# Kernel tuning notes

Hardware: AMD Instinct MI355X
Metric: run time of the kernel (lower is better)

The kernel has to match this reference:

```python
import jax, jax.numpy as jnp
import numpy as np

N_NODES = 20000
N_EDGES = 160000
N_GRAPHS = 64
EMB_DIM = 16
N_BASIS = 16
MAX_RADIUS = 5.0
MUL_IN = 8   # output_size: multiplicity of scalar atom features
MUL_OUT = 4  # multiplicity per output irrep (4x0e + 4x1o + 4x2e -> dim 36)
W_NUMEL = 3 * MUL_IN * MUL_IN * MUL_OUT  # 768 per-edge tensor-product weights


def setup_inputs() -> dict:
    key = jax.random.key(0)
    ks = jax.random.split(key, 16)
    pos = jax.random.normal(ks[0], (N_NODES, 3), jnp.float32) * 3.0
    A = jax.random.randint(ks[1], (N_NODES,), 0, 10)
    batch = jnp.sort(jax.random.randint(ks[2], (N_NODES,), 0, N_GRAPHS))
    edge_src = jax.random.randint(ks[3], (N_EDGES,), 0, N_NODES)
    edge_dst = jax.random.randint(ks[4], (N_EDGES,), 0, N_NODES)
    edge_shifts = jnp.zeros((N_EDGES, 3), jnp.float32)
    cell = jnp.broadcast_to(jnp.eye(3, dtype=jnp.float32) * 10.0, (N_GRAPHS, 3, 3))
    emb_table = jax.random.normal(ks[5], (10, EMB_DIM), jnp.float32)
    fit_w1 = jax.random.normal(ks[6], (EMB_DIM, 64), jnp.float32) * (2.0 / EMB_DIM) ** 0.5
    fit_b1 = jnp.zeros((64,), jnp.float32)
    fit_w2 = jax.random.normal(ks[7], (64, 32), jnp.float32) * (2.0 / 64.0) ** 0.5
    fit_b2 = jnp.zeros((32,), jnp.float32)
    fit_w3 = jax.random.normal(ks[8], (32, MUL_IN), jnp.float32) * (2.0 / 32.0) ** 0.5
    fit_b3 = jnp.zeros((MUL_IN,), jnp.float32)
    fc_w1 = jax.random.normal(ks[9], (N_BASIS, 64), jnp.float32)
    fc_w2 = jax.random.normal(ks[10], (64, 64), jnp.float32)
    fc_w3 = jax.random.normal(ks[11], (64, 64), jnp.float32)
    fc_w4 = jax.random.normal(ks[12], (64, W_NUMEL), jnp.float32)
    return dict(pos=pos, A=A, batch=batch, edge_src=edge_src, edge_dst=edge_dst,
                edge_shifts=edge_shifts, cell=cell, emb_table=emb_table,
                fit_w1=fit_w1, fit_b1=fit_b1, fit_w2=fit_w2, fit_b2=fit_b2,
                fit_w3=fit_w3, fit_b3=fit_b3,
                fc_w1=fc_w1, fc_w2=fc_w2, fc_w3=fc_w3, fc_w4=fc_w4)


def _forward(pos, edge_shifts, cell, emb_table, fit_w1, fit_b1, fit_w2, fit_b2,
             fit_w3, fit_b3, fc_w1, fc_w2, fc_w3, fc_w4, A, batch, edge_src, edge_dst):
    E = edge_src.shape[0]
    # edge vectors with periodic shifts
    shift = jnp.einsum('ni,nij->nj', edge_shifts, cell[batch[edge_src]])
    ev = pos[edge_dst] - pos[edge_src] + shift                     # [E,3]
    r = jnp.sqrt(jnp.sum(ev * ev, axis=1))                         # [E]
    v = ev / jnp.maximum(r, 1e-9)[:, None]
    x, y, z = v[:, 0], v[:, 1], v[:, 2]
    # spherical harmonics lmax=2, normalize=True, 'component' normalization (e3nn order)
    sh0 = jnp.ones_like(x)                                         # [E]
    sh1 = jnp.sqrt(3.0) * jnp.stack([y, z, x], axis=-1)            # [E,3]
    s15 = jnp.sqrt(15.0); s5 = jnp.sqrt(5.0)
    sh2 = jnp.stack([s15 * x * y, s15 * y * z, (s5 / 2.0) * (3.0 * z * z - 1.0),
                     s15 * x * z, (s15 / 2.0) * (x * x - y * y)], axis=-1)  # [E,5]
    # node scalar features: embedding + fitnet MLP (SiLU)
    h = jax.nn.silu(emb_table[A] @ fit_w1 + fit_b1)
    h = jax.nn.silu(h @ fit_w2 + fit_b2)
    Ai = h @ fit_w3 + fit_b3                                       # [N, MUL_IN]
    # soft_one_hot_linspace(gaussian, cutoff=True) * sqrt(n_basis)
    centers = jnp.linspace(0.0, MAX_RADIUS, N_BASIS + 2)[1:-1]
    step = centers[1] - centers[0]
    rb = jnp.exp(-(((r[:, None] - centers) / step) ** 2)) / 1.12 * jnp.sqrt(jnp.float32(N_BASIS))
    # radial net -> per-edge tensor-product weights (e3nn FullyConnectedNet style, no bias)
    g = jax.nn.silu(rb @ fc_w1 / jnp.sqrt(jnp.float32(N_BASIS)))
    g = jax.nn.silu(g @ fc_w2 / 8.0)
    g = jax.nn.silu(g @ fc_w3 / 8.0)
    w = (g @ fc_w4 / 8.0).reshape(E, 3, MUL_IN, MUL_IN, MUL_OUT)   # [E,3 paths,u,v,w]
    # FullTensorProduct(Ai_src, sh) then FullyConnectedTensorProduct(., Ai_dst) with
    # per-edge weights; scalar x irrep paths factorize: out_l[e,w,m] = S_l[e,w]*sh_l[e,m]
    P = Ai[edge_src][:, :, None] * Ai[edge_dst][:, None, :]        # [E,u,v]
    S = jnp.einsum('euv,eluvw->elw', P, w) / jnp.float32(MUL_IN)   # path norm 1/sqrt(u*v)
    out0 = S[:, 0, :] * sh0[:, None]                               # [E,4]
    out1 = (S[:, 1, :, None] * sh1[:, None, :]).reshape(E, MUL_OUT * 3)
    out2 = (S[:, 2, :, None] * sh2[:, None, :]).reshape(E, MUL_OUT * 5)
    ef = jnp.concatenate([out0, out1, out2], axis=-1)              # [E,36]
    # scatter-mean to destination nodes
    cnt = jnp.clip(jax.ops.segment_sum(jnp.ones((E,), ef.dtype), edge_dst,
                                       num_segments=N_NODES), 1.0)
    return jax.ops.segment_sum(ef, edge_dst, num_segments=N_NODES) / cnt[:, None]


def reference(pos, A, batch, edge_src, edge_dst, edge_shifts, cell, emb_table,
              fit_w1, fit_b1, fit_w2, fit_b2, fit_w3, fit_b3,
              fc_w1, fc_w2, fc_w3, fc_w4):
    return _forward(pos, edge_shifts, cell, emb_table, fit_w1, fit_b1, fit_w2,
                    fit_b2, fit_w3, fit_b3, fc_w1, fc_w2, fc_w3, fc_w4,
                    A, batch, edge_src, edge_dst)
```

## Files before the change

kernel.cpp:

```cpp
#include <hip/hip_runtime.h>
#include <math.h>

#define N_NODES 20000
#define N_EDGES 160000

#define NBINS   512
#define BINS1   513
#define RMAX    7.5f

static const size_t OFF_T   = 0;
static const size_t OFF_G   = OFF_T   + (size_t)100 * 64 * 12 * 4;
static const size_t OFF_SV  = OFF_G   + (size_t)64 * BINS1 * 4;
static const size_t OFF_NOFF= OFF_SV  + (size_t)100 * BINS1 * 12 * 4;
static const size_t OFF_NCNT= OFF_NOFF+ (size_t)(N_NODES + 1) * 4;
static const size_t OFF_RANK= OFF_NCNT+ (size_t)N_NODES * 4;
static const size_t OFF_CSR = OFF_RANK+ (size_t)N_EDGES * 4;

#define P1_T_BLOCKS  25
#define P1_G_BLOCKS  9
#define P1_H_BLOCKS  625
#define P1_GRID (P1_T_BLOCKS + P1_G_BLOCKS + P1_H_BLOCKS)
#define P2_SCAN_BLOCKS 79
#define P2_CHUNKS 9
#define P2_GRID (P2_SCAN_BLOCKS + 100 * P2_CHUNKS)

__device__ __forceinline__ float silu_f(float x) {
    return x / (1.0f + __expf(-x));
}

__global__ __launch_bounds__(256) void prep1_kernel(
        const float* __restrict__ emb,
        const float* __restrict__ fw1, const float* __restrict__ fb1,
        const float* __restrict__ fw2, const float* __restrict__ fb2,
        const float* __restrict__ fw3, const float* __restrict__ fb3,
        const float* __restrict__ fc_w1, const float* __restrict__ fc_w2,
        const float* __restrict__ fc_w3, const float* __restrict__ fc_w4,
        const int* __restrict__ edst,
        float* __restrict__ T, float* __restrict__ g_tT,
        int* __restrict__ cnt_i, int* __restrict__ rank_e) {
    __shared__ float smem[4096];
    int b = blockIdx.x;
    int tid = threadIdx.x;

    if (b < P1_T_BLOCKS) {
        float* h1s = smem;
        float* h2s = smem + 640;
        float* ai  = smem + 960;
        for (int idx = tid; idx < 640; idx += 256) {
            int t = idx >> 6, j = idx & 63;
            float acc = fb1[j];
            #pragma unroll
            for (int i = 0; i < 16; i++) acc += emb[t * 16 + i] * fw1[i * 64 + j];
            h1s[idx] = silu_f(acc);
        }
        __syncthreads();
        for (int idx = tid; idx < 320; idx += 256) {
            int t = idx >> 5, j = idx & 31;
            float acc = fb2[j];
            #pragma unroll
            for (int i = 0; i < 64; i++) acc += h1s[t * 64 + i] * fw2[i * 32 + j];
            h2s[idx] = silu_f(acc);
        }
        __syncthreads();
        if (tid < 80) {
            int t = tid >> 3, j = tid & 7;
            float acc = fb3[j];
            #pragma unroll
            for (int i = 0; i < 32; i++) acc += h2s[t * 32 + i] * fw3[i * 8 + j];
            ai[tid] = acc;
        }
        __syncthreads();

        int idx = b * 256 + tid;
        int pair = idx >> 6;
        int k = idx & 63;
        int ts = pair / 10, td = pair - ts * 10;
        float a[8], bb[8];
        #pragma unroll
        for (int i = 0; i < 8; i++) a[i] = ai[ts * 8 + i];
        #pragma unroll
        for (int i = 0; i < 8; i++) bb[i] = ai[td * 8 + i];
        float sv[12];
        #pragma unroll
        for (int i = 0; i < 12; i++) sv[i] = 0.0f;
        const float* wk = fc_w4 + k * 768;
        #pragma unroll 2
        for (int u = 0; u < 8; u++) {
            #pragma unroll
            for (int v = 0; v < 8; v++) {
                float ab = a[u] * bb[v];
                const float* wp = wk + u * 32 + v * 4;
                float4 w0 = *(const float4*)(wp);
                float4 w1 = *(const float4*)(wp + 256);
                float4 w2 = *(const float4*)(wp + 512);
                sv[0] += ab * w0.x; sv[1] += ab * w0.y; sv[2]  += ab * w0.z; sv[3]  += ab * w0.w;
                sv[4] += ab * w1.x; sv[5] += ab * w1.y; sv[6]  += ab * w1.z; sv[7]  += ab * w1.w;
                sv[8] += ab * w2.x; sv[9] += ab * w2.y; sv[10] += ab * w2.z; sv[11] += ab * w2.w;
            }
        }
        float* tp = T + pair * 768 + k * 12;
        #pragma unroll
        for (int j = 0; j < 12; j++) tp[j] = sv[j];
    } else if (b < P1_T_BLOCKS + P1_G_BLOCKS) {
        int lane = tid & 63;
        int wq = __builtin_amdgcn_readfirstlane(tid >> 6);
        int bin = (b - P1_T_BLOCKS) * 64 + lane;
        bool valid = (bin <= NBINS);
        float r = (float)bin * (RMAX / (float)NBINS);

        float rb[16];
        const float step = 5.0f / 17.0f;
        const float istep = 17.0f / 5.0f;
        const float rsc = 4.0f / 1.12f;
        #pragma unroll
        for (int i = 0; i < 16; i++) {
            float dd = (r - (float)(i + 1) * step) * istep;
            rb[i] = __expf(-dd * dd) * rsc;
        }

        #pragma unroll
        for (int jj = 0; jj < 16; jj++) {
            int j = wq * 16 + jj;
            float a0 = 0, a1 = 0, a2 = 0, a3 = 0;
            #pragma unroll
            for (int i = 0; i < 16; i += 4) {
                a0 += rb[i]     * fc_w1[(i)     * 64 + j];
                a1 += rb[i + 1] * fc_w1[(i + 1) * 64 + j];
                a2 += rb[i + 2] * fc_w1[(i + 2) * 64 + j];
                a3 += rb[i + 3] * fc_w1[(i + 3) * 64 + j];
            }
            smem[j * 64 + lane] = silu_f(((a0 + a1) + (a2 + a3)) * 0.25f);
        }
        __syncthreads();

        float acc[16];
        #pragma unroll
        for (int jj = 0; jj < 16; jj++) acc[jj] = 0.0f;
        #pragma unroll
        for (int c = 0; c < 4; c++) {
            float hc[16];
            #pragma unroll
            for (int i = 0; i < 16; i++) hc[i] = smem[(c * 16 + i) * 64 + lane];
            #pragma unroll
            for (int jj = 0; jj < 16; jj++) {
                int j = wq * 16 + jj;
                #pragma unroll
                for (int i = 0; i < 16; i++) acc[jj] += hc[i] * fc_w2[(c * 16 + i) * 64 + j];
            }
        }
        __syncthreads();
        #pragma unroll
        for (int jj = 0; jj < 16; jj++) smem[(wq * 16 + jj) * 64 + lane] = silu_f(acc[jj] * 0.125f);
        __syncthreads();

        #pragma unroll
        for (int jj = 0; jj < 16; jj++) acc[jj] = 0.0f;
        #pragma unroll
        for (int c = 0; c < 4; c++) {
            float hc[16];
            #pragma unroll
            for (int i = 0; i < 16; i++) hc[i] = smem[(c * 16 + i) * 64 + lane];
            #pragma unroll
            for (int jj = 0; jj < 16; jj++) {
                int j = wq * 16 + jj;
                #pragma unroll
                for (int i = 0; i < 16; i++) acc[jj] += hc[i] * fc_w3[(c * 16 + i) * 64 + j];
            }
        }
        if (valid) {
            #pragma unroll
            for (int jj = 0; jj < 16; jj++)
                g_tT[(size_t)(wq * 16 + jj) * BINS1 + bin] = silu_f(acc[jj] * 0.125f);
        }
    } else {
        int e = (b - P1_T_BLOCKS - P1_G_BLOCKS) * 256 + tid;
        if (e < N_EDGES) rank_e[e] = atomicAdd(&cnt_i[edst[e]], 1);
    }
}

__global__ __launch_bounds__(256) void prep2_kernel(
        const int* __restrict__ cnt_i, int* __restrict__ node_off,
        const float* __restrict__ T, const float* __restrict__ g_tT,
        float* __restrict__ sv_table) {
    __shared__ float smem[4096];
    int b = blockIdx.x;
    int tid = threadIdx.x;

    if (b < P2_SCAN_BLOCKS) {
        int* wred = (int*)smem;
        int* wsum = (int*)smem + 4;
        int lane = tid & 63, w = tid >> 6;
        int nbase = b * 256;
        int n = nbase + tid;
        int c = (n < N_NODES) ? cnt_i[n] : 0;

        int part = 0;
        for (int i = tid; i < nbase; i += 256) part += cnt_i[i];
        #pragma unroll
        for (int off = 1; off < 64; off <<= 1) part += __shfl_xor(part, off);
        if (lane == 0) wred[w] = part;

        int sc = c;
        #pragma unroll
        for (int off = 1; off < 64; off <<= 1) {
            int v2 = __shfl_up(sc, off);
            if (lane >= off) sc += v2;
        }
        if (lane == 63) wsum[w] = sc;
        __syncthreads();

        int base = wred[0] + wred[1] + wred[2] + wred[3];
        int wb = 0;
        #pragma unroll
        for (int i = 0; i < 4; i++) wb += (i < w) ? wsum[i] : 0;
        if (n < N_NODES) node_off[n] = base + wb + (sc - c);
        if (b == 0 && tid == 0) node_off[N_NODES] = N_EDGES;
        return;
    }

    int idx = b - P2_SCAN_BLOCKS;
    int pair = idx / P2_CHUNKS;
    int chunk = idx - pair * P2_CHUNKS;

    float* part = smem;
    float* Tlds = smem + 3328;

    const float* Tp = T + pair * 768;
    #pragma unroll
    for (int i = tid; i < 768; i += 256) Tlds[i] = Tp[i];
    __syncthreads();

    int lane = tid & 63;
    int wq = tid >> 6;
    int bin = chunk * 64 + lane;
    bool valid = (bin <= NBINS);
    int rb = valid ? bin : NBINS;

    float acc[12];
    #pragma unroll
    for (int j = 0; j < 12; j++) acc[j] = 0.0f;
    #pragma unroll
    for (int kk = 0; kk < 16; kk++) {
        int k = wq * 16 + kk;
        float g = g_tT[(size_t)k * BINS1 + rb];
        const float* Tl = Tlds + k * 12;
        #pragma unroll
        for (int j = 0; j < 12; j++) acc[j] += g * Tl[j];
    }

    float* pp = part + (size_t)wq * 64 * 13 + (size_t)lane * 13;
    #pragma unroll
    for (int j = 0; j < 12; j++) pp[j] = acc[j];
    __syncthreads();

    const float isc = 1.0f / 64.0f;
    float* svp = sv_table + (size_t)pair * BINS1 * 12 + (size_t)chunk * 64 * 12;
    #pragma unroll
    for (int i = 0; i < 3; i++) {
        int o = tid + 256 * i;
        int bl = o / 12;
        int j = o - bl * 12;
        if (chunk * 64 + bl <= NBINS) {
            float s = part[(size_t)0 * 832 + bl * 13 + j]
                    + part[(size_t)1 * 832 + bl * 13 + j]
                    + part[(size_t)2 * 832 + bl * 13 + j]
                    + part[(size_t)3 * 832 + bl * 13 + j];
            svp[o] = s * isc;
        }
    }
}

__global__ __launch_bounds__(256) void csr_kernel(
        const int* __restrict__ edst, const int* __restrict__ rank_e,
        const int* __restrict__ node_off, int* __restrict__ csr_eid) {
    int e = blockIdx.x * 256 + threadIdx.x;
    if (e >= N_EDGES) return;
    csr_eid[node_off[edst[e]] + rank_e[e]] = e;
}

__global__ __launch_bounds__(256) void gather_kernel(
        const float* __restrict__ pos, const int* __restrict__ batch,
        const int* __restrict__ esrc, const float* __restrict__ shifts,
        const float* __restrict__ cell, const int* __restrict__ A,
        const int* __restrict__ node_off, const int* __restrict__ csr_eid,
        const float* __restrict__ sv_table, float* __restrict__ out) {
    int t = blockIdx.x * 256 + threadIdx.x;
    if (t >= N_NODES * 8) return;
    int n = t >> 3;
    int q = t & 7;
    int beg = node_off[n], end = node_off[n + 1];

    float pdx = pos[n * 3 + 0], pdy = pos[n * 3 + 1], pdz = pos[n * 3 + 2];
    int Ad = A[n];

    const float S3  = 1.7320508075688772f;
    const float S15 = 3.8729833462074170f;
    const float S5  = 2.2360679774997896f;

    float acc[36];
    #pragma unroll
    for (int j = 0; j < 36; j++) acc[j] = 0.0f;

    for (int p = beg + q; p < end; p += 8) {
        int e = csr_eid[p];
        int s = esrc[e];
        int gb = batch[s];
        float t0 = shifts[e * 3 + 0], t1 = shifts[e * 3 + 1], t2 = shifts[e * 3 + 2];
        const float* C = cell + gb * 9;
        float shx = t0 * C[0] + t1 * C[3] + t2 * C[6];
        float shy = t0 * C[1] + t1 * C[4] + t2 * C[7];
        float shz = t0 * C[2] + t1 * C[5] + t2 * C[8];
        float ex = pdx - pos[s * 3 + 0] + shx;
        float ey = pdy - pos[s * 3 + 1] + shy;
        float ez = pdz - pos[s * 3 + 2] + shz;
        float r = sqrtf(ex * ex + ey * ey + ez * ez);
        float inv = 1.0f / fmaxf(r, 1e-9f);
        float x = ex * inv, y = ey * inv, z = ez * inv;

        float sv[12];
        if (r >= RMAX) {
            #pragma unroll
            for (int j = 0; j < 12; j++) sv[j] = 0.0f;
        } else {
            int pair = A[s] * 10 + Ad;
            float tt = r * ((float)NBINS / RMAX);
            int i = (int)tt;
            i = (i > NBINS - 1) ? (NBINS - 1) : i;
            float f = tt - (float)i;
            const float* r0 = sv_table + ((size_t)pair * BINS1 + i) * 12;
            #pragma unroll
            for (int j = 0; j < 12; j++) {
                float lo = r0[j], hi = r0[12 + j];
                sv[j] = lo + f * (hi - lo);
            }
        }

        float sh1v[3] = { S3 * y, S3 * z, S3 * x };
        float sh2v[5] = { S15 * x * y, S15 * y * z, 0.5f * S5 * (3.0f * z * z - 1.0f),
                          S15 * x * z, 0.5f * S15 * (x * x - y * y) };

        acc[0] += sv[0]; acc[1] += sv[1]; acc[2] += sv[2]; acc[3] += sv[3];
        #pragma unroll
        for (int w = 0; w < 4; w++) {
            float sw = sv[4 + w];
            #pragma unroll
            for (int j = 0; j < 3; j++) acc[4 + w * 3 + j] += sw * sh1v[j];
        }
        #pragma unroll
        for (int w = 0; w < 4; w++) {
            float sw = sv[8 + w];
            #pragma unroll
            for (int j = 0; j < 5; j++) acc[16 + w * 5 + j] += sw * sh2v[j];
        }
    }

    #pragma unroll
    for (int j = 0; j < 36; j++) {
        acc[j] += __shfl_xor(acc[j], 1);
        acc[j] += __shfl_xor(acc[j], 2);
        acc[j] += __shfl_xor(acc[j], 4);
    }

    if (q == 0) {
        float c = 1.0f / fmaxf((float)(end - beg), 1.0f);
        float4* o4 = (float4*)out + (size_t)n * 9;
        #pragma unroll
        for (int k = 0; k < 9; k++)
            o4[k] = make_float4(acc[k * 4 + 0] * c, acc[k * 4 + 1] * c,
                                acc[k * 4 + 2] * c, acc[k * 4 + 3] * c);
    }
}

extern "C" void kernel_launch(void* const* d_in, const int* in_sizes, int n_in,
                              void* d_out, int out_size, void* d_ws, size_t ws_size,
                              hipStream_t stream) {
    const float* pos    = (const float*)d_in[0];
    const int*   A      = (const int*)d_in[1];
    const int*   batch  = (const int*)d_in[2];
    const int*   esrc   = (const int*)d_in[3];
    const int*   edst   = (const int*)d_in[4];
    const float* shifts = (const float*)d_in[5];
    const float* cell   = (const float*)d_in[6];
    const float* emb    = (const float*)d_in[7];
    const float* fw1    = (const float*)d_in[8];
    const float* fb1    = (const float*)d_in[9];
    const float* fw2    = (const float*)d_in[10];
    const float* fb2    = (const float*)d_in[11];
    const float* fw3    = (const float*)d_in[12];
    const float* fb3    = (const float*)d_in[13];
    const float* fcw1   = (const float*)d_in[14];
    const float* fcw2   = (const float*)d_in[15];
    const float* fcw3   = (const float*)d_in[16];
    const float* fcw4   = (const float*)d_in[17];
    float* out = (float*)d_out;

    char* ws = (char*)d_ws;
    float* T       = (float*)(ws + OFF_T);
    float* g_tT    = (float*)(ws + OFF_G);
    float* sv_table= (float*)(ws + OFF_SV);
    int*   node_off= (int*)(ws + OFF_NOFF);
    int*   cnt_i   = (int*)(ws + OFF_NCNT);
    int*   rank_e  = (int*)(ws + OFF_RANK);
    int*   csr_eid = (int*)(ws + OFF_CSR);

    hipMemsetAsync(cnt_i, 0, (size_t)N_NODES * 4, stream);

    prep1_kernel<<<P1_GRID, 256, 0, stream>>>(emb, fw1, fb1, fw2, fb2, fw3, fb3,
                                              fcw1, fcw2, fcw3, fcw4, edst,
                                              T, g_tT, cnt_i, rank_e);
    prep2_kernel<<<P2_GRID, 256, 0, stream>>>(cnt_i, node_off, T, g_tT, sv_table);
    csr_kernel<<<(N_EDGES + 255) / 256, 256, 0, stream>>>(edst, rank_e, node_off, csr_eid);
    gather_kernel<<<(N_NODES * 8 + 255) / 256, 256, 0, stream>>>(
        pos, batch, esrc, shifts, cell, A, node_off, csr_eid, sv_table, out);
}
```

Measured before the change: 157.3 us.

## Stage per-edge source position and species into CSR order before gather

Replaces the CSR edge-id scatter with a staging kernel. Each edge's shifted source position and source species are written as a float4 at its sorted slot. The gather kernel then reads one contiguous float4 per edge instead of chasing edge id, source index, batch, cell, pos and A through indirect loads. Lanes per node also rise from 8 to 16, with one extra shuffle stage. In exchange the workspace write per edge grows to 16 bytes, and most lanes sit idle for nodes with few edges.

```diff
diff --git a/kernel.cpp b/kernel.cpp
--- a/kernel.cpp
+++ b/kernel.cpp
@@ -14,7 +14,7 @@
 static const size_t OFF_NOFF= OFF_SV  + (size_t)100 * BINS1 * 12 * 4;
 static const size_t OFF_NCNT= OFF_NOFF+ (size_t)(N_NODES + 1) * 4;
 static const size_t OFF_RANK= OFF_NCNT+ (size_t)N_NODES * 4;
-static const size_t OFF_CSR = OFF_RANK+ (size_t)N_EDGES * 4;
+static const size_t OFF_STG = OFF_RANK+ (size_t)N_EDGES * 4;
 
 #define P1_T_BLOCKS  25
 #define P1_G_BLOCKS  9
@@ -270,24 +270,38 @@
     }
 }
 
-__global__ __launch_bounds__(256) void csr_kernel(
-        const int* __restrict__ edst, const int* __restrict__ rank_e,
-        const int* __restrict__ node_off, int* __restrict__ csr_eid) {
+__global__ __launch_bounds__(256) void stage_kernel(
+        const float* __restrict__ pos, const int* __restrict__ batch,
+        const int* __restrict__ esrc, const int* __restrict__ edst,
+        const float* __restrict__ shifts, const float* __restrict__ cell,
+        const int* __restrict__ A,
+        const int* __restrict__ node_off, const int* __restrict__ rank_e,
+        float4* __restrict__ staged) {
     int e = blockIdx.x * 256 + threadIdx.x;
     if (e >= N_EDGES) return;
-    csr_eid[node_off[edst[e]] + rank_e[e]] = e;
+
+    int s = esrc[e], d = edst[e];
+    int slot = node_off[d] + rank_e[e];
+    int gb = batch[s];
+    float t0 = shifts[e * 3 + 0], t1 = shifts[e * 3 + 1], t2 = shifts[e * 3 + 2];
+    const float* C = cell + gb * 9;
+    float shx = t0 * C[0] + t1 * C[3] + t2 * C[6];
+    float shy = t0 * C[1] + t1 * C[4] + t2 * C[7];
+    float shz = t0 * C[2] + t1 * C[5] + t2 * C[8];
+    float qx = pos[s * 3 + 0] - shx;
+    float qy = pos[s * 3 + 1] - shy;
+    float qz = pos[s * 3 + 2] - shz;
+    staged[slot] = make_float4(qx, qy, qz, __int_as_float(A[s]));
 }
 
 __global__ __launch_bounds__(256) void gather_kernel(
-        const float* __restrict__ pos, const int* __restrict__ batch,
-        const int* __restrict__ esrc, const float* __restrict__ shifts,
-        const float* __restrict__ cell, const int* __restrict__ A,
-        const int* __restrict__ node_off, const int* __restrict__ csr_eid,
+        const float* __restrict__ pos, const int* __restrict__ A,
+        const int* __restrict__ node_off, const float4* __restrict__ staged,
         const float* __restrict__ sv_table, float* __restrict__ out) {
     int t = blockIdx.x * 256 + threadIdx.x;
-    if (t >= N_NODES * 8) return;
-    int n = t >> 3;
-    int q = t & 7;
+    if (t >= N_NODES * 16) return;
+    int n = t >> 4;
+    int q = t & 15;
     int beg = node_off[n], end = node_off[n + 1];
 
     float pdx = pos[n * 3 + 0], pdy = pos[n * 3 + 1], pdz = pos[n * 3 + 2];
@@ -301,18 +315,12 @@
     #pragma unroll
     for (int j = 0; j < 36; j++) acc[j] = 0.0f;
 
-    for (int p = beg + q; p < end; p += 8) {
-        int e = csr_eid[p];
-        int s = esrc[e];
-        int gb = batch[s];
-        float t0 = shifts[e * 3 + 0], t1 = shifts[e * 3 + 1], t2 = shifts[e * 3 + 2];
-        const float* C = cell + gb * 9;
-        float shx = t0 * C[0] + t1 * C[3] + t2 * C[6];
-        float shy = t0 * C[1] + t1 * C[4] + t2 * C[7];
-        float shz = t0 * C[2] + t1 * C[5] + t2 * C[8];
-        float ex = pdx - pos[s * 3 + 0] + shx;
-        float ey = pdy - pos[s * 3 + 1] + shy;
-        float ez = pdz - pos[s * 3 + 2] + shz;
+    for (int p = beg + q; p < end; p += 16) {
+        float4 rec = staged[p];
+        float ex = pdx - rec.x;
+        float ey = pdy - rec.y;
+        float ez = pdz - rec.z;
+        int As = __float_as_int(rec.w);
         float r = sqrtf(ex * ex + ey * ey + ez * ez);
         float inv = 1.0f / fmaxf(r, 1e-9f);
         float x = ex * inv, y = ey * inv, z = ez * inv;
@@ -322,7 +330,7 @@
             #pragma unroll
             for (int j = 0; j < 12; j++) sv[j] = 0.0f;
         } else {
-            int pair = A[s] * 10 + Ad;
+            int pair = As * 10 + Ad;
             float tt = r * ((float)NBINS / RMAX);
             int i = (int)tt;
             i = (i > NBINS - 1) ? (NBINS - 1) : i;
@@ -359,6 +367,7 @@
         acc[j] += __shfl_xor(acc[j], 1);
         acc[j] += __shfl_xor(acc[j], 2);
         acc[j] += __shfl_xor(acc[j], 4);
+        acc[j] += __shfl_xor(acc[j], 8);
     }
 
     if (q == 0) {
@@ -401,7 +410,7 @@
     int*   node_off= (int*)(ws + OFF_NOFF);
     int*   cnt_i   = (int*)(ws + OFF_NCNT);
     int*   rank_e  = (int*)(ws + OFF_RANK);
-    int*   csr_eid = (int*)(ws + OFF_CSR);
+    float4* staged = (float4*)(ws + OFF_STG);
 
     hipMemsetAsync(cnt_i, 0, (size_t)N_NODES * 4, stream);
 
@@ -409,7 +418,8 @@
                                               fcw1, fcw2, fcw3, fcw4, edst,
                                               T, g_tT, cnt_i, rank_e);
     prep2_kernel<<<P2_GRID, 256, 0, stream>>>(cnt_i, node_off, T, g_tT, sv_table);
-    csr_kernel<<<(N_EDGES + 255) / 256, 256, 0, stream>>>(edst, rank_e, node_off, csr_eid);
-    gather_kernel<<<(N_NODES * 8 + 255) / 256, 256, 0, stream>>>(
-        pos, batch, esrc, shifts, cell, A, node_off, csr_eid, sv_table, out);
-}
+    stage_kernel<<<(N_EDGES + 255) / 256, 256, 0, stream>>>(
+        pos, batch, esrc, edst, shifts, cell, A, node_off, rank_e, staged);
+    gather_kernel<<<(N_NODES * 16 + 255) / 256, 256, 0, stream>>>(
+        pos, A, node_off, staged, sv_table, out);
+}
```

New measurement: 162.3 us. 3.2% more time.
